# Kernel optimization log

Hardware: AMD Instinct MI355X
Metric: run time of the kernel (lower is better)

The kernel has to match this reference:

```python
import jax, jax.numpy as jnp
from jax import lax
import numpy as np

LEVELS = 17
VAR_N = 4
UNITS = 3 * LEVELS          # 51 neurons: motor 17, command 13, inter 21
MOTOR = LEVELS
PRED_N = 4
UNFOLDS = 6                 # ncps LTC default ode_unfolds
EPS = 1e-8
B = 32768                   # recurrence length = B + PRED_N
D = VAR_N * LEVELS          # 68


def _build_wiring(seed=0):
    # AutoNCP(51, 17, sparsity_level=0.8): inter=21, command=13, motor=17
    # sensory_fanout=4, inter_fanout=2, 5 recurrent command synapses, motor_fanin=2
    rng = np.random.default_rng(seed)
    motor, command, S = 17, 13, LEVELS
    N = UNITS
    cmd = np.arange(motor, motor + command)
    intr = np.arange(motor + command, N)
    adj = np.zeros((N, N), np.float32)
    sadj = np.zeros((S, N), np.float32)
    pol = lambda: float(rng.choice([-1.0, 1.0]))
    for s in range(S):
        for d in rng.choice(intr, 4, replace=False):
            sadj[s, d] = pol()
    for d in intr:
        if not sadj[:, d].any():
            sadj[int(rng.integers(S)), d] = pol()
    for i in intr:
        for d in rng.choice(cmd, 2, replace=False):
            adj[i, d] = pol()
    for d in cmd:
        if not adj[intr, d].any():
            adj[int(rng.choice(intr)), d] = pol()
    for _ in range(5):
        adj[int(rng.choice(cmd)), int(rng.choice(cmd))] = pol()
    for m in range(motor):
        for srci in rng.choice(cmd, 2, replace=False):
            adj[srci, m] = pol()
    return adj, sadj


def setup_inputs():
    key = jax.random.key(0)
    ks = iter(jax.random.split(key, 48))
    u = lambda s, lo, hi: jax.random.uniform(next(ks), s, jnp.float32, lo, hi)
    lin = lambda i, o: jax.random.normal(next(ks), (i, o), jnp.float32) * (i ** -0.5)
    adj, sadj = _build_wiring()
    V, N, S = VAR_N, UNITS, LEVELS
    M1 = (LEVELS + D) // 2           # 42
    G = VAR_N * D                    # 272
    G2 = (G + D) // 2                # 170
    return dict(
        x=jax.random.normal(next(ks), (B, D), jnp.float32),
        pre_w1=lin(D, D), pre_b1=jnp.zeros((D,), jnp.float32),
        pre_w2=lin(D, D), pre_b2=jnp.zeros((D,), jnp.float32),
        gleak=u((V, N), 0.001, 1.0), vleak=u((V, N), -0.2, 0.2), cm=u((V, N), 0.4, 0.6),
        w=u((V, N, N), 0.001, 1.0), sigma=u((V, N, N), 3.0, 8.0), mu=u((V, N, N), 0.3, 0.8),
        erev=jnp.asarray(np.tile(adj, (V, 1, 1))),
        sens_w=u((V, S, N), 0.001, 1.0), sens_sigma=u((V, S, N), 3.0, 8.0), sens_mu=u((V, S, N), 0.3, 0.8),
        sens_erev=jnp.asarray(np.tile(sadj, (V, 1, 1))),
        in_w=jnp.ones((V, S), jnp.float32), in_b=jnp.zeros((V, S), jnp.float32),
        out_w=jnp.ones((V, MOTOR), jnp.float32), out_b=jnp.zeros((V, MOTOR), jnp.float32),
        tW1=lin(LEVELS, LEVELS), tb1=jnp.zeros((LEVELS,), jnp.float32),
        tW2=lin(LEVELS, M1), tb2=jnp.zeros((M1,), jnp.float32),
        tW3=lin(M1, D), tb3=jnp.zeros((D,), jnp.float32),
        gW1=lin(G, G), gb1=jnp.zeros((G,), jnp.float32),
        gW2=lin(G, G2), gb2=jnp.zeros((G2,), jnp.float32),
        gW3=lin(G2, D), gb3=jnp.zeros((D,), jnp.float32),
        mask=jnp.asarray((adj != 0).astype(np.float32)),
        sens_mask=jnp.asarray((sadj != 0).astype(np.float32)),
    )


def _forward(x, pre_w1, pre_b1, pre_w2, pre_b2,
             gleak, vleak, cm, w, sigma, mu, erev,
             sens_w, sens_sigma, sens_mu, sens_erev,
             in_w, in_b, out_w, out_b,
             tW1, tb1, tW2, tb2, tW3, tb3,
             gW1, gb1, gW2, gb2, gW3, gb3,
             mask, sens_mask, ckpt=False):
    sig = jax.nn.sigmoid
    # VarEncoder: Linear -> Sigmoid -> Linear
    h = sig(x @ pre_w1 + pre_b1) @ pre_w2 + pre_b2                  # (B, 68)
    xs = h.reshape(-1, VAR_N, LEVELS).transpose(1, 0, 2)            # (V, B, 17)
    seqs = jnp.concatenate([xs, jnp.repeat(xs[:, -1:, :], PRED_N, axis=1)], axis=1)  # (V, T, 17)

    def run(p, seq):
        gl_, vl_, cm_, w_, sg_, mu_, er_, sw_, ssg_, smu_, ser_, iw_, ib_, ow_, ob_ = p
        gl = jax.nn.softplus(gl_)                 # (N,)
        wp = jax.nn.softplus(w_) * mask           # (N, N) sparse NCP wiring
        swp = jax.nn.softplus(sw_) * sens_mask    # (S, N)
        cmt = jax.nn.softplus(cm_) * UNFOLDS      # cm / (elapsed=1 / unfolds)

        def step(v, u_in):
            u = u_in * iw_ + ib_                                   # affine input mapping
            sact = swp * sig((u[:, None] - smu_) * ssg_)           # (S, N)
            num_s = (sact * ser_).sum(0)
            den_s = sact.sum(0)

            def unfold(vv, _):
                wa = wp * sig((vv[:, None] - mu_) * sg_)           # (N, N), src axis 0
                vv = (cmt * vv + gl * vl_ + (wa * er_).sum(0) + num_s) / (
                    cmt + gl + wa.sum(0) + den_s + EPS)
                return vv, None

            v, _ = lax.scan(unfold, v, None, length=UNFOLDS)
            return v, v[:MOTOR] * ow_ + ob_                        # affine output mapping

        stepf = jax.checkpoint(step) if ckpt else step
        _, outs = lax.scan(stepf, jnp.zeros((UNITS,), seq.dtype), seq)
        return outs                                                # (T, 17)

    p = (gleak, vleak, cm, w, sigma, mu, erev,
         sens_w, sens_sigma, sens_mu, sens_erev, in_w, in_b, out_w, out_b)
    rs = jax.vmap(run, in_axes=(0, 0))(p, seqs)                    # (V, T, 17)
    r = rs.transpose(1, 0, 2)                                      # (T, V, 17)
    # CrossConnector: per-tile MLP 17->17->42->68 (sigmoids), flatten, 272->272->170->68
    t = sig(sig(sig(r @ tW1 + tb1) @ tW2 + tb2) @ tW3 + tb3)        # (T, V, 68)
    g = t.reshape(t.shape[0], -1)                                   # (T, 272)
    return sig(sig(g @ gW1 + gb1) @ gW2 + gb2) @ gW3 + gb3          # (T, 68)


def reference(x, pre_w1, pre_b1, pre_w2, pre_b2,
              gleak, vleak, cm, w, sigma, mu, erev,
              sens_w, sens_sigma, sens_mu, sens_erev,
              in_w, in_b, out_w, out_b,
              tW1, tb1, tW2, tb2, tW3, tb3,
              gW1, gb1, gW2, gb2, gW3, gb3,
              mask, sens_mask):
    return _forward(x, pre_w1, pre_b1, pre_w2, pre_b2,
                    gleak, vleak, cm, w, sigma, mu, erev,
                    sens_w, sens_sigma, sens_mu, sens_erev,
                    in_w, in_b, out_w, out_b,
                    tW1, tb1, tW2, tb2, tW3, tb3,
                    gW1, gb1, gW2, gb2, gW3, gb3,
                    mask, sens_mask)
```

## Files before the change

### kernel.cpp

```cpp
#include <hip/hip_runtime.h>
#include <hip/hip_bf16.h>
#include <math.h>

#define LEVELS 17
#define VARN   4
#define UNITS  51
#define MOTOR  17
#define NB     32768
#define TT     (NB + 4)
#define DD     68
#define LOG2E  1.4426950408889634f
#define TROWS  16

#define W_WARM  10
#define L_CHUNK 34
#define NCHUNK  ((TT + L_CHUNK - 1) / L_CHUNK)

#define W_F     64
#define L_F     64
#define NCHUNK_F ((TT + L_F - 1) / L_F)
#define CAP_R  16

#define MROWS  48
#define MBLK   ((TT + MROWS - 1) / MROWS)
#define EBLK   ((NB + MROWS - 1) / MROWS)
#define BUFSZ  (48 * 272 + 64)
#define EBUFSZ (48 * 72 + 64)

#define OFF_WA 0
#define OFF_WB 7680
#define OFF_WC 24576
#define OFF_WD 76800
#define OFF_WE 155136
#define OFF_WF 205824
#define OFF_P1 221184
#define OFF_P2 228864
#define WTS_SHORTS 236544
#define PSENS_N (VARN * LEVELS * UNITS)

typedef __attribute__((ext_vector_type(8))) short short8v;
typedef __attribute__((ext_vector_type(4))) float f32x4;

__device__ __forceinline__ float fast_rcp(float x) { return __builtin_amdgcn_rcpf(x); }
__device__ __forceinline__ float fast_exp2(float x) { return __builtin_amdgcn_exp2f(x); }
__device__ __forceinline__ float sigf(float x) { return fast_rcp(1.0f + __expf(-x)); }
__device__ __forceinline__ float softplusf(float x) { return logf(1.0f + expf(x)); }
__device__ __forceinline__ unsigned short f2bf(float x) {
    unsigned int u = __float_as_uint(x);
    unsigned int r = u + 0x7FFFu + ((u >> 16) & 1u);
    return (unsigned short)(r >> 16);
}

__global__ __launch_bounds__(256) void prep_weights(
    const float* __restrict__ tW1, const float* __restrict__ tW2, const float* __restrict__ tW3,
    const float* __restrict__ gW1, const float* __restrict__ gW2, const float* __restrict__ gW3,
    const float* __restrict__ pW1, const float* __restrict__ pW2,
    unsigned short* __restrict__ wts)
{
    const int ph = blockIdx.y;
    const int KTt[8]   = {3, 3, 6, 9, 9, 6, 3, 3};
    const int NCt[8]   = {5, 11, 17, 17, 11, 5, 5, 5};
    const int offsT[8] = {OFF_WA, OFF_WB, OFF_WC, OFF_WD, OFF_WE, OFF_WF, OFF_P1, OFF_P2};
    int S = NCt[ph] * KTt[ph] * 512;
    int idx = blockIdx.x * 256 + threadIdx.x;
    if (idx >= S) return;
    int tile = idx >> 9;
    int r    = idx & 511;
    int lane = r >> 3;
    int e    = r & 7;
    int KTp  = KTt[ph];
    int ct   = tile / KTp;
    int kt   = tile - ct * KTp;
    int n = ct * 16 + (lane & 15);
    int k = kt * 32 + (lane >> 4) * 8 + e;
    float val = 0.0f;
    switch (ph) {
        case 0: if (k < 68 && n < 68) { int v = k / 17; if (n / 17 == v) val = tW1[(k % 17) * 17 + (n % 17)]; } break;
        case 1: if (k < 68 && n < 168) { int v = k / 17; int c = n - 42 * v; if (c >= 0 && c < 42) val = tW2[(k % 17) * 42 + c]; } break;
        case 2: if (k < 168 && n < 272) { int v = k / 42; int c = n - 68 * v; if (c >= 0 && c < 68) val = tW3[(k % 42) * 68 + c]; } break;
        case 3: if (k < 272 && n < 272) val = gW1[k * 272 + n]; break;
        case 4: if (k < 272 && n < 170) val = gW2[k * 170 + n]; break;
        case 5: if (k < 170 && n < 68)  val = gW3[k * 68 + n]; break;
        case 6: if (k < 68 && n < 68)   val = pW1[k * 68 + n]; break;
        case 7: if (k < 68 && n < 68)   val = pW2[k * 68 + n]; break;
    }
    wts[offsT[ph] + idx] = f2bf(val);
}

__global__ __launch_bounds__(256) void prep_sens(
    const float* __restrict__ sens_w, const float* __restrict__ sens_sigma,
    const float* __restrict__ sens_mu, const float* __restrict__ sens_erev,
    float4* __restrict__ psens)
{
    int idx = blockIdx.x * 256 + threadIdx.x;
    if (idx >= PSENS_N) return;
    float sg = sens_sigma[idx], m = sens_mu[idx];
    float wf = softplusf(sens_w[idx]);
    psens[idx] = make_float4(fast_exp2(sg * m * LOG2E), -sg * LOG2E, wf, wf * sens_erev[idx]);
}

template<int KT, int NC>
__device__ __forceinline__ void mfma_phase(
    const unsigned short* __restrict__ wt,
    const unsigned short* __restrict__ bufIn, int ldkIn,
    unsigned short* __restrict__ bufOut, int ldkOut,
    const float* __restrict__ bias, int bmod, int Nvalid,
    int lane, int wave)
{
    #pragma unroll
    for (int rt = 0; rt < 3; ++rt) {
        short8v af[KT];
        int abase = (rt * 16 + (lane & 15)) * ldkIn + 8 * (lane >> 4);
        #pragma unroll
        for (int kt = 0; kt < KT; ++kt)
            af[kt] = *reinterpret_cast<const short8v*>(&bufIn[abase + kt * 32]);
        for (int ct = wave; ct < NC; ct += 4) {
            int c = ct * 16 + (lane & 15);
            const unsigned short* wp = wt + (size_t)(ct * KT) * 512 + lane * 8;
            short8v bf[KT];
            #pragma unroll
            for (int kt = 0; kt < KT; ++kt)
                bf[kt] = *reinterpret_cast<const short8v*>(&wp[kt * 512]);
            f32x4 acc = {0.0f, 0.0f, 0.0f, 0.0f};
            #pragma unroll
            for (int kt = 0; kt < KT; ++kt)
                acc = __builtin_amdgcn_mfma_f32_16x16x32_bf16(af[kt], bf[kt], acc, 0, 0, 0);
            float bv = 0.0f;
            if (c < Nvalid) {
                int cb = (bmod == 0) ? (c % 17) : (bmod == 1) ? (c % 42) : (bmod == 2) ? (c % 68) : c;
                bv = bias[cb];
            }
            #pragma unroll
            for (int i = 0; i < 4; ++i) {
                float vv = sigf(acc[i] + bv);
                int rl = rt * 16 + (lane >> 4) * 4 + i;
                if (c < ldkOut) bufOut[rl * ldkOut + c] = f2bf(vv);
            }
        }
    }
}

template<int KT>
__device__ __forceinline__ void mfma_final(
    const unsigned short* __restrict__ wt,
    const unsigned short* __restrict__ bufIn, int ldkIn,
    float* __restrict__ io, int baseRow,
    const float* __restrict__ gb3, int lane, int wave)
{
    #pragma unroll
    for (int rt = 0; rt < 3; ++rt) {
        short8v af[KT];
        int abase = (rt * 16 + (lane & 15)) * ldkIn + 8 * (lane >> 4);
        #pragma unroll
        for (int kt = 0; kt < KT; ++kt)
            af[kt] = *reinterpret_cast<const short8v*>(&bufIn[abase + kt * 32]);
        for (int ct = wave; ct < 5; ct += 4) {
            int c = ct * 16 + (lane & 15);
            const unsigned short* wp = wt + (size_t)(ct * KT) * 512 + lane * 8;
            short8v bf[KT];
            #pragma unroll
            for (int kt = 0; kt < KT; ++kt)
                bf[kt] = *reinterpret_cast<const short8v*>(&wp[kt * 512]);
            f32x4 acc = {0.0f, 0.0f, 0.0f, 0.0f};
            #pragma unroll
            for (int kt = 0; kt < KT; ++kt)
                acc = __builtin_amdgcn_mfma_f32_16x16x32_bf16(af[kt], bf[kt], acc, 0, 0, 0);
            float bv = (c < 68) ? gb3[c] : 0.0f;
            #pragma unroll
            for (int i = 0; i < 4; ++i) {
                int row = baseRow + rt * 16 + (lane >> 4) * 4 + i;
                if (c < 68 && row < TT) io[(size_t)row * DD + c] = acc[i] + bv;
            }
        }
    }
}

__global__ __launch_bounds__(256) void mlp_mfma(
    float* __restrict__ io, const unsigned short* __restrict__ wts,
    const float* __restrict__ tb1, const float* __restrict__ tb2, const float* __restrict__ tb3,
    const float* __restrict__ gb1, const float* __restrict__ gb2, const float* __restrict__ gb3)
{
    __shared__ unsigned short buf0[BUFSZ];
    __shared__ unsigned short buf1[BUFSZ];
    int tid = threadIdx.x, lane = tid & 63, wave = tid >> 6;
    int baseRow = blockIdx.x * MROWS;

    for (int e = tid; e < BUFSZ; e += 256) { buf0[e] = 0; buf1[e] = 0; }
    __syncthreads();
    for (int e = tid; e < MROWS * DD; e += 256) {
        int r = e / DD, c = e % DD;
        int gr = baseRow + r;
        float xv = (gr < TT) ? io[(size_t)gr * DD + c] : 0.0f;
        buf0[r * 72 + c] = f2bf(xv);
    }
    __syncthreads();
    mfma_phase<3, 5 >(wts + OFF_WA, buf0, 72,  buf1, 72,  tb1, 0, 68,  lane, wave); __syncthreads();
    mfma_phase<3, 11>(wts + OFF_WB, buf1, 72,  buf0, 168, tb2, 1, 168, lane, wave); __syncthreads();
    mfma_phase<6, 17>(wts + OFF_WC, buf0, 168, buf1, 272, tb3, 2, 272, lane, wave); __syncthreads();
    mfma_phase<9, 17>(wts + OFF_WD, buf1, 272, buf0, 272, gb1, 3, 272, lane, wave); __syncthreads();
    mfma_phase<9, 11>(wts + OFF_WE, buf0, 272, buf1, 176, gb2, 3, 170, lane, wave); __syncthreads();
    mfma_final<6>(wts + OFF_WF, buf1, 176, io, baseRow, gb3, lane, wave);
}

__global__ __launch_bounds__(256) void enc_mfma(
    const float* __restrict__ x, const unsigned short* __restrict__ wts,
    const float* __restrict__ pb1, const float* __restrict__ pb2,
    float* __restrict__ seq)
{
    __shared__ unsigned short buf0[EBUFSZ];
    __shared__ unsigned short buf1[EBUFSZ];
    int tid = threadIdx.x, lane = tid & 63, wave = tid >> 6;
    int baseRow = blockIdx.x * MROWS;

    for (int e = tid; e < EBUFSZ; e += 256) { buf0[e] = 0; buf1[e] = 0; }
    __syncthreads();
    for (int e = tid; e < MROWS * DD; e += 256) {
        int r = e / DD, c = e % DD;
        int gr = baseRow + r;
        float xv = (gr < NB) ? x[(size_t)gr * DD + c] : 0.0f;
        buf0[r * 72 + c] = f2bf(xv);
    }
    __syncthreads();
    mfma_phase<3, 5>(wts + OFF_P1, buf0, 72, buf1, 72, pb1, 3, 68, lane, wave);
    __syncthreads();
    #pragma unroll
    for (int rt = 0; rt < 3; ++rt) {
        short8v af[3];
        int abase = (rt * 16 + (lane & 15)) * 72 + 8 * (lane >> 4);
        #pragma unroll
        for (int kt = 0; kt < 3; ++kt)
            af[kt] = *reinterpret_cast<const short8v*>(&buf1[abase + kt * 32]);
        for (int ct = wave; ct < 5; ct += 4) {
            int c = ct * 16 + (lane & 15);
            const unsigned short* wp = wts + OFF_P2 + (size_t)(ct * 3) * 512 + lane * 8;
            short8v bf[3];
            #pragma unroll
            for (int kt = 0; kt < 3; ++kt)
                bf[kt] = *reinterpret_cast<const short8v*>(&wp[kt * 512]);
            f32x4 acc = {0.0f, 0.0f, 0.0f, 0.0f};
            #pragma unroll
            for (int kt = 0; kt < 3; ++kt)
                acc = __builtin_amdgcn_mfma_f32_16x16x32_bf16(af[kt], bf[kt], acc, 0, 0, 0);
            float bv = (c < 68) ? pb2[c] : 0.0f;
            #pragma unroll
            for (int i = 0; i < 4; ++i) {
                int row = baseRow + rt * 16 + (lane >> 4) * 4 + i;
                if (c < 68 && row < NB) {
                    float vv = acc[i] + bv;
                    int v = c / 17, s = c % 17;
                    float* dst = seq + ((size_t)v * TT + row) * LEVELS + s;
                    dst[0] = vv;
                    if (row == NB - 1) {
                        dst[1 * LEVELS] = vv; dst[2 * LEVELS] = vv;
                        dst[3 * LEVELS] = vv; dst[4 * LEVELS] = vv;
                    }
                }
            }
        }
    }
}

#define SENS_TPW 16
__global__ __launch_bounds__(256) void sens_kernel(
    const float* __restrict__ seq,
    const float4* __restrict__ psens,
    const float* __restrict__ in_w, const float* __restrict__ in_b,
    const float* __restrict__ sens_mask,
    float2* __restrict__ tab)
{
    int gwi = blockIdx.x * 4 + (threadIdx.x >> 6);
    int j   = threadIdx.x & 63;
    int v    = gwi & 3;
    int tbase = (gwi >> 2) * SENS_TPW;
    if (tbase >= TT) return;

    unsigned int bits0 = 0;
    if (j < UNITS)
        for (int s = 0; s < LEVELS; ++s)
            bits0 |= (sens_mask[s * UNITS + j] != 0.0f ? 1u : 0u) << s;
    int ns = __popc(bits0);
    int mS = ns;
    #pragma unroll
    for (int off = 32; off; off >>= 1) mS = max(mS, __shfl_xor(mS, off, 64));

    float iw = (j < LEVELS) ? in_w[v * LEVELS + j] : 0.0f;
    float ib = (j < LEVELS) ? in_b[v * LEVELS + j] : 0.0f;

    int tend = min(TT, tbase + SENS_TPW);
    for (int t = tbase; t < tend; ++t) {
        float u = (j < LEVELS)
            ? fmaf(seq[((size_t)v * TT + t) * LEVELS + j], iw, ib) : 0.0f;
        unsigned int bits = bits0;
        float num = 0.0f, den = 0.0f;
        for (int k = 0; k < mS; ++k) {
            bool on = (k < ns) && (bits != 0u);
            int s = on ? (__ffs(bits) - 1) : 0;
            if (on) bits &= bits - 1;
            float us = __shfl(u, s, 64);
            float4 p = psens[(v * LEVELS + s) * UNITS + (j < UNITS ? j : 0)];
            float g = fast_rcp(fmaf(p.x, fast_exp2(p.y * us), 1.0f));
            if (on) { num = fmaf(p.w, g, num); den = fmaf(p.z, g, den); }
        }
        if (j < UNITS)
            tab[((size_t)v * TT + t) * UNITS + j] = make_float2(num, den);
    }
}

template<int MH>
__device__ void scan_body3(
    int j, int jnS, int jnV, float ownMul, float helpMul, int h1, int h2,
    int myStart, int myCnt, bool isH1,
    unsigned long long colbits, int v, int t0, int wstart, int tend,
    float cmt, float glvl, float cgl, float ow, float ob,
    const float* __restrict__ w, const float* __restrict__ sigma,
    const float* __restrict__ mu, const float* __restrict__ erev,
    const float2* __restrict__ tab, float* __restrict__ rout)
{
    int   src[MH]; float fw[MH], fc[MH], fk[MH], fwfe[MH];
    unsigned long long bits = colbits;
    for (int s = 0; s < myStart; ++s) bits &= bits - 1;
    #pragma unroll
    for (int k = 0; k < MH; ++k) {
        bool on = (k < myCnt);
        int sc = on ? (__ffsll((unsigned long long)bits) - 1) : 0;
        src[k] = sc;
        size_t pi = ((size_t)v * UNITS + sc) * UNITS + jnS;
        float sg = on ? sigma[pi] : 0.0f;
        float m  = on ? mu[pi]    : 0.0f;
        fw[k] = on ? softplusf(w[pi]) : 0.0f;
        fc[k] = fast_exp2(sg * m * LOG2E);
        fk[k] = -sg * LOG2E;
        fwfe[k] = on ? fw[k] * erev[pi] : 0.0f;
        if (on) bits &= bits - 1;
    }
    const float2* tp = tab + (size_t)v * TT * UNITS + jnV;
    float* rp = rout + (size_t)v * LEVELS + j;
    float2 nd = tp[(size_t)t0 * UNITS];
    float vreg = 0.0f;
    for (int t = t0; t < tend; ++t) {
        float2 ndc = nd;
        if (t + 1 < tend) nd = tp[(size_t)(t + 1) * UNITS];
        float bn = isH1 ? 0.0f : (glvl + ndc.x);
        float bd = isH1 ? 1.0f : (cgl + ndc.y);
        #pragma unroll
        for (int uf = 0; uf < 6; ++uf) {
            float vs[MH];
            #pragma unroll
            for (int k = 0; k < MH; ++k) vs[k] = __shfl(vreg, src[k], 64);
            float accn = 0.0f, accd = 0.0f;
            #pragma unroll
            for (int k = 0; k < MH; ++k) {
                float g = fast_rcp(fmaf(fc[k], fast_exp2(fk[k] * vs[k]), 1.0f));
                accn = fmaf(fwfe[k], g, accn);
                accd = fmaf(fw[k], g, accd);
            }
            float p1n = __shfl(accn, h1, 64);
            float p1d = __shfl(accd, h1, 64);
            float p2n = __shfl(accn, h2, 64);
            float p2d = __shfl(accd, h2, 64);
            float num = fmaf(accn, ownMul, bn) + helpMul * (p1n + p2n);
            float den = fmaf(accd, ownMul, bd) + helpMul * (p1d + p2d);
            vreg = fmaf(cmt, vreg, num) * fast_rcp(den);
        }
        if (j < MOTOR && t >= wstart) rp[(size_t)t * DD] = fmaf(vreg, ow, ob);
    }
}

__device__ void scan_body_gen(
    int j, int jn, bool hasHelp, int partner, int myStart, int myCnt, int mcMax,
    unsigned long long colbits, int v, int t0, int wstart, int tend,
    float cmt, float glvl, float cgl, float ow, float ob, bool isHelper,
    const float* __restrict__ w, const float* __restrict__ sigma,
    const float* __restrict__ mu, const float* __restrict__ erev,
    const float2* __restrict__ tab, float* __restrict__ rout)
{
    unsigned long long mybits = colbits;
    for (int s = 0; s < myStart; ++s) mybits &= mybits - 1;
    const float2* tp = tab + (size_t)v * TT * UNITS + jn;
    float* rp = rout + (size_t)v * LEVELS + j;
    float vreg = 0.0f;
    for (int t = t0; t < tend; ++t) {
        float2 ndc = tp[(size_t)t * UNITS];
        float bn = isHelper ? 0.0f : (glvl + ndc.x);
        float bd = isHelper ? 0.0f : (cgl + ndc.y);
        for (int uf = 0; uf < 6; ++uf) {
            unsigned long long bits = mybits;
            float num = bn, den = bd;
            for (int k = 0; k < mcMax; ++k) {
                bool on = (k < myCnt) && (bits != 0ull);
                int sc = on ? (__ffsll(bits) - 1) : 0;
                if (on) bits &= bits - 1;
                float vs = __shfl(vreg, sc, 64);
                size_t pi = ((size_t)v * UNITS + sc) * UNITS + jn;
                float a = on ? softplusf(w[pi]) * sigf((vs - mu[pi]) * sigma[pi]) : 0.0f;
                num = fmaf(a, on ? erev[pi] : 0.0f, num);
                den += a;
            }
            float pn = __shfl(num, partner, 64);
            float pd = __shfl(den, partner, 64);
            if (hasHelp) { num += pn; den += pd; }
            vreg = fmaf(cmt, vreg, num) * fast_rcp(den);
        }
        if (j < MOTOR && t >= wstart) rp[(size_t)t * DD] = fmaf(vreg, ow, ob);
    }
}

__global__ __launch_bounds__(256, 8) void scan_pre(
    const float2* __restrict__ tab,
    const float* __restrict__ gleak, const float* __restrict__ vleak, const float* __restrict__ cm,
    const float* __restrict__ w, const float* __restrict__ sigma,
    const float* __restrict__ mu, const float* __restrict__ erev,
    const float* __restrict__ out_w, const float* __restrict__ out_b,
    const float* __restrict__ mask,
    float* __restrict__ rout)
{
    int gwi = (blockIdx.x << 2) + (threadIdx.x >> 6);
    int j = threadIdx.x & 63;
    int v = gwi & 3;
    int chunk = gwi >> 2;
    if (chunk >= NCHUNK) return;
    int wstart = chunk * L_CHUNK;
    int tend = min(TT, wstart + L_CHUNK);
    int t0 = max(0, wstart - W_WARM);

    bool isH1   = (j >= UNITS);
    bool isH2   = (j >= 30 && j < 43);
    bool isCmdL = (j >= MOTOR && j < 30);
    int jnV = isH1 ? (j - 34) : j;
    int jnS = isH1 ? (j - 34) : (isH2 ? (j - 13) : j);

    unsigned long long colbits = 0ull;
    for (int i = 0; i < UNITS; ++i)
        colbits |= (unsigned long long)(mask[i * UNITS + jnS] != 0.0f ? 1 : 0) << i;
    int nf = __popcll(colbits);

    int ownIn = 0;
    if (j >= 30 && j < UNITS) {
        for (int i = 0; i < UNITS; ++i)
            ownIn |= (mask[i * UNITS + j] != 0.0f ? 1 : 0);
    }
    int bad = ownIn;
    #pragma unroll
    for (int off = 32; off; off >>= 1) bad |= __shfl_xor(bad, off, 64);

    int n1 = (nf + 2) / 3;
    int n2 = (nf - n1 + 1) / 2;
    int n3 = nf - n1 - n2;
    int myStart, myCnt;
    if (isH1)        { myStart = n1 + n2; myCnt = n3; }
    else if (isH2)   { myStart = n1;      myCnt = n2; }
    else if (isCmdL) { myStart = 0;       myCnt = n1; }
    else             { myStart = 0;       myCnt = nf; }
    float ownMul  = (isH1 || isH2) ? 0.0f : 1.0f;
    float helpMul = isCmdL ? 1.0f : 0.0f;
    int h1 = isCmdL ? (j + 34) : j;
    int h2 = isCmdL ? (j + 13) : j;

    float cmt  = softplusf(cm[v * UNITS + jnV]) * 6.0f;
    float gl   = softplusf(gleak[v * UNITS + jnV]);
    float glvl = gl * vleak[v * UNITS + jnV];
    float cgl  = cmt + gl + 1e-8f;
    float ow = (j < MOTOR) ? out_w[v * LEVELS + j] : 0.0f;
    float ob = (j < MOTOR) ? out_b[v * LEVELS + j] : 0.0f;

    int mc = myCnt;
    #pragma unroll
    for (int off = 32; off; off >>= 1) mc = max(mc, __shfl_xor(mc, off, 64));

    if (!bad && mc <= 2)
        scan_body3<2>(j, jnS, jnV, ownMul, helpMul, h1, h2, myStart, myCnt, isH1,
                      colbits, v, t0, wstart, tend, cmt, glvl, cgl, ow, ob,
                      w, sigma, mu, erev, tab, rout);
    else if (!bad && mc <= 3)
        scan_body3<3>(j, jnS, jnV, ownMul, helpMul, h1, h2, myStart, myCnt, isH1,
                      colbits, v, t0, wstart, tend, cmt, glvl, cgl, ow, ob,
                      w, sigma, mu, erev, tab, rout);
    else if (!bad && mc <= 4)
        scan_body3<4>(j, jnS, jnV, ownMul, helpMul, h1, h2, myStart, myCnt, isH1,
                      colbits, v, t0, wstart, tend, cmt, glvl, cgl, ow, ob,
                      w, sigma, mu, erev, tab, rout);
    else {
        int jn = isH1 ? (j - 34) : j;
        unsigned long long cb = 0ull;
        for (int i = 0; i < UNITS; ++i)
            cb |= (unsigned long long)(mask[i * UNITS + jn] != 0.0f ? 1 : 0) << i;
        int nfg = __popcll(cb);
        bool isCmd = (jn >= MOTOR && jn < 30);
        int nh = (nfg + 1) >> 1;
        int gs, gc;
        if (isH1)      { gs = nh; gc = nfg - nh; }
        else if (isCmd){ gs = 0;  gc = nh; }
        else           { gs = 0;  gc = nfg; }
        bool hasHelp = (!isH1) && isCmd;
        int partner = hasHelp ? (jn + 34) : j;
        float cmtg  = softplusf(cm[v * UNITS + jn]) * 6.0f;
        float glg   = softplusf(gleak[v * UNITS + jn]);
        float glvlg = glg * vleak[v * UNITS + jn];
        float cglg  = cmtg + glg + 1e-8f;
        int mg = gc;
        #pragma unroll
        for (int off = 32; off; off >>= 1) mg = max(mg, __shfl_xor(mg, off, 64));
        scan_body_gen(j, jn, hasHelp, partner, gs, gc, mg, cb, v, t0, wstart, tend,
                      cmtg, glvlg, cglg, ow, ob, isH1, w, sigma, mu, erev, tab, rout);
    }
}

__global__ __launch_bounds__(128) void enc_kernel(
    const float* __restrict__ x,
    const float* __restrict__ W1, const float* __restrict__ b1,
    const float* __restrict__ W2, const float* __restrict__ b2,
    float* __restrict__ seq)
{
    int t = blockIdx.x;
    int j = threadIdx.x;
    __shared__ float xs[DD];
    __shared__ float h1[DD];
    if (j < DD) xs[j] = x[(size_t)t * DD + j];
    __syncthreads();
    if (j < DD) {
        float acc = b1[j];
        #pragma unroll 4
        for (int k = 0; k < DD; ++k) acc = fmaf(xs[k], W1[k * DD + j], acc);
        h1[j] = sigf(acc);
    }
    __syncthreads();
    if (j < DD) {
        float acc = b2[j];
        #pragma unroll 4
        for (int k = 0; k < DD; ++k) acc = fmaf(h1[k], W2[k * DD + j], acc);
        int v = j / LEVELS, s = j % LEVELS;
        float* dst = seq + ((size_t)v * TT + t) * LEVELS + s;
        dst[0] = acc;
        if (t == NB - 1) {
            dst[1 * LEVELS] = acc; dst[2 * LEVELS] = acc;
            dst[3 * LEVELS] = acc; dst[4 * LEVELS] = acc;
        }
    }
}

template<int MF, int MS>
__device__ __forceinline__ void scan_loop_f(
    int j, int v, int t0, int wstart, int tend,
    const float* __restrict__ seq, float* __restrict__ rout,
    float cmt, float glvl, float cgl, float iw, float ib, float ow, float ob,
    int nf, int ns,
    const int* rs_, const float* rw_, const float* rc_, const float* rk_, const float* re_,
    const int* ss_, const float* sw_, const float* sc_, const float* sk_, const float* se_)
{
    int fs[MF]; float fw[MF], fc[MF], fk[MF], fe[MF];
    #pragma unroll
    for (int k = 0; k < MF; ++k) {
        bool on = k < nf;
        int idx = j * CAP_R + k;
        fs[k] = on ? rs_[idx] : 0;
        fw[k] = on ? rw_[idx] : 0.0f;
        fc[k] = on ? rc_[idx] : 1.0f;
        fk[k] = on ? rk_[idx] : 0.0f;
        fe[k] = on ? re_[idx] : 0.0f;
    }
    int gs[MS]; float gw[MS], gc[MS], gk[MS], ge[MS];
    #pragma unroll
    for (int k = 0; k < MS; ++k) {
        bool on = k < ns;
        int idx = j * LEVELS + k;
        gs[k] = on ? ss_[idx] : 0;
        gw[k] = on ? sw_[idx] : 0.0f;
        gc[k] = on ? sc_[idx] : 1.0f;
        gk[k] = on ? sk_[idx] : 0.0f;
        ge[k] = on ? se_[idx] : 0.0f;
    }
    const float* sp = seq + (size_t)v * TT * LEVELS + j;
    float* rp = rout + (size_t)v * LEVELS + j;
    float xnext = (j < LEVELS) ? sp[(size_t)t0 * LEVELS] : 0.0f;
    float vreg = 0.0f;
    for (int t = t0; t < tend; ++t) {
        float u = fmaf(xnext, iw, ib);
        if (j < LEVELS && t + 1 < tend) xnext = sp[(size_t)(t + 1) * LEVELS];
        float us[MS];
        #pragma unroll
        for (int k = 0; k < MS; ++k) us[k] = __shfl(u, gs[k], 64);
        float sa[MS];
        #pragma unroll
        for (int k = 0; k < MS; ++k)
            sa[k] = gw[k] * fast_rcp(fmaf(gc[k], fast_exp2(gk[k] * us[k]), 1.0f));
        float bn = glvl, bd = cgl;
        #pragma unroll
        for (int k = 0; k < MS; ++k) { bn = fmaf(sa[k], ge[k], bn); bd += sa[k]; }
        #pragma unroll
        for (int uf = 0; uf < 6; ++uf) {
            float vsa[MF];
            #pragma unroll
            for (int k = 0; k < MF; ++k) vsa[k] = __shfl(vreg, fs[k], 64);
            float aa[MF];
            #pragma unroll
            for (int k = 0; k < MF; ++k)
                aa[k] = fw[k] * fast_rcp(fmaf(fc[k], fast_exp2(fk[k] * vsa[k]), 1.0f));
            float num = bn, den = bd;
            #pragma unroll
            for (int k = 0; k < MF; ++k) { num = fmaf(aa[k], fe[k], num); den += aa[k]; }
            vreg = fmaf(cmt, vreg, num) * fast_rcp(den);
        }
        if (j < LEVELS && t >= wstart) rp[(size_t)t * DD] = fmaf(vreg, ow, ob);
    }
}

__global__ __launch_bounds__(64) void scan_fallback(
    const float* __restrict__ seq,
    const float* __restrict__ gleak, const float* __restrict__ vleak, const float* __restrict__ cm,
    const float* __restrict__ w, const float* __restrict__ sigma,
    const float* __restrict__ mu, const float* __restrict__ erev,
    const float* __restrict__ sens_w, const float* __restrict__ sens_sigma,
    const float* __restrict__ sens_mu, const float* __restrict__ sens_erev,
    const float* __restrict__ in_w, const float* __restrict__ in_b,
    const float* __restrict__ out_w, const float* __restrict__ out_b,
    const float* __restrict__ mask, const float* __restrict__ sens_mask,
    float* __restrict__ rout)
{
    __shared__ int   rs_[UNITS * CAP_R];
    __shared__ float rw_[UNITS * CAP_R], rc_[UNITS * CAP_R], rk_[UNITS * CAP_R], re_[UNITS * CAP_R];
    __shared__ int   ss_[UNITS * LEVELS];
    __shared__ float sw_[UNITS * LEVELS], sc_[UNITS * LEVELS], sk_[UNITS * LEVELS], se_[UNITS * LEVELS];
    __shared__ int   cnts[64], scnts[64];
    __shared__ int   red[2];

    int j = threadIdx.x;
    int v = blockIdx.x & 3;
    int chunk = blockIdx.x >> 2;
    int wstart = chunk * L_F;
    if (wstart >= TT) return;
    int tend = min(TT, wstart + L_F);
    int t0 = max(0, wstart - W_F);

    int nf = 0, ns = 0;
    if (j < UNITS) {
        for (int i = 0; i < UNITS; ++i) {
            if (mask[i * UNITS + j] != 0.0f) {
                if (nf < CAP_R) {
                    size_t pi = ((size_t)v * UNITS + i) * UNITS + j;
                    int idx = j * CAP_R + nf;
                    float sg = sigma[pi], m = mu[pi];
                    rs_[idx] = i;
                    rw_[idx] = softplusf(w[pi]);
                    rc_[idx] = fast_exp2(sg * m * LOG2E);
                    rk_[idx] = -sg * LOG2E;
                    re_[idx] = erev[pi];
                }
                nf++;
            }
        }
        for (int s = 0; s < LEVELS; ++s) {
            if (sens_mask[s * UNITS + j] != 0.0f) {
                size_t pi = ((size_t)v * LEVELS + s) * UNITS + j;
                int idx = j * LEVELS + ns;
                float sg = sens_sigma[pi], m = sens_mu[pi];
                ss_[idx] = s;
                sw_[idx] = softplusf(sens_w[pi]);
                sc_[idx] = fast_exp2(sg * m * LOG2E);
                sk_[idx] = -sg * LOG2E;
                se_[idx] = sens_erev[pi];
                ns++;
            }
        }
    }
    cnts[j] = nf; scnts[j] = ns;
    __syncthreads();
    if (j == 0) {
        int mf = 0, ms = 0;
        for (int i = 0; i < UNITS; ++i) { mf = max(mf, cnts[i]); ms = max(ms, scnts[i]); }
        red[0] = mf; red[1] = ms;
    }
    __syncthreads();
    int maxF = red[0], maxS = red[1];

    int jc = (j < UNITS) ? j : (UNITS - 1);
    float cmt  = softplusf(cm[v * UNITS + jc]) * 6.0f;
    float gl   = softplusf(gleak[v * UNITS + jc]);
    float glvl = gl * vleak[v * UNITS + jc];
    float cgl  = cmt + gl + 1e-8f;
    float iw = (j < LEVELS) ? in_w[v * LEVELS + j]  : 0.0f;
    float ib = (j < LEVELS) ? in_b[v * LEVELS + j]  : 0.0f;
    float ow = (j < LEVELS) ? out_w[v * LEVELS + j] : 0.0f;
    float ob = (j < LEVELS) ? out_b[v * LEVELS + j] : 0.0f;

    if (maxF <= 11 && maxS <= 12)
        scan_loop_f<11, 12>(j, v, t0, wstart, tend, seq, rout, cmt, glvl, cgl, iw, ib, ow, ob, nf, ns,
                            rs_, rw_, rc_, rk_, re_, ss_, sw_, sc_, sk_, se_);
    else
        scan_loop_f<16, 17>(j, v, t0, wstart, tend, seq, rout, cmt, glvl, cgl, iw, ib, ow, ob, nf, ns,
                            rs_, rw_, rc_, rk_, re_, ss_, sw_, sc_, sk_, se_);
}

__global__ __launch_bounds__(256) void mlp_kernel(
    float* __restrict__ io,
    const float* __restrict__ tW1, const float* __restrict__ tb1,
    const float* __restrict__ tW2, const float* __restrict__ tb2,
    const float* __restrict__ tW3, const float* __restrict__ tb3,
    const float* __restrict__ gW1, const float* __restrict__ gb1,
    const float* __restrict__ gW2, const float* __restrict__ gb2,
    const float* __restrict__ gW3, const float* __restrict__ gb3)
{
    __shared__ __align__(16) float A[TROWS][272];
    __shared__ __align__(16) float Bf[TROWS][272];
    int base = blockIdx.x * TROWS;
    int tid = threadIdx.x;

    for (int e = tid; e < TROWS * DD; e += 256) {
        int r = e / DD, c = e % DD;
        A[r][c] = (base + r < TT) ? io[(size_t)(base + r) * DD + c] : 0.0f;
    }
    __syncthreads();
    for (int c = tid; c < 4 * LEVELS; c += 256) {
        int vv = c / LEVELS, cc = c % LEVELS;
        float acc[TROWS]; float bias = tb1[cc];
        #pragma unroll
        for (int r = 0; r < TROWS; ++r) acc[r] = bias;
        for (int k = 0; k < LEVELS; ++k) {
            float wv = tW1[k * LEVELS + cc];
            #pragma unroll
            for (int r = 0; r < TROWS; ++r) acc[r] = fmaf(A[r][vv * LEVELS + k], wv, acc[r]);
        }
        #pragma unroll
        for (int r = 0; r < TROWS; ++r) Bf[r][c] = sigf(acc[r]);
    }
    __syncthreads();
    for (int c = tid; c < 4 * 42; c += 256) {
        int vv = c / 42, cc = c % 42;
        float acc[TROWS]; float bias = tb2[cc];
        #pragma unroll
        for (int r = 0; r < TROWS; ++r) acc[r] = bias;
        for (int k = 0; k < LEVELS; ++k) {
            float wv = tW2[k * 42 + cc];
            #pragma unroll
            for (int r = 0; r < TROWS; ++r) acc[r] = fmaf(Bf[r][vv * LEVELS + k], wv, acc[r]);
        }
        #pragma unroll
        for (int r = 0; r < TROWS; ++r) A[r][vv * 42 + cc] = sigf(acc[r]);
    }
    __syncthreads();
    for (int c = tid; c < 4 * DD; c += 256) {
        int vv = c / DD, cc = c % DD;
        float acc[TROWS]; float bias = tb3[cc];
        #pragma unroll
        for (int r = 0; r < TROWS; ++r) acc[r] = bias;
        for (int k = 0; k < 42; ++k) {
            float wv = tW3[k * DD + cc];
            #pragma unroll
            for (int r = 0; r < TROWS; ++r) acc[r] = fmaf(A[r][vv * 42 + k], wv, acc[r]);
        }
        #pragma unroll
        for (int r = 0; r < TROWS; ++r) Bf[r][c] = sigf(acc[r]);
    }
    __syncthreads();
    for (int c = tid; c < 272; c += 256) {
        float acc[TROWS]; float bias = gb1[c];
        #pragma unroll
        for (int r = 0; r < TROWS; ++r) acc[r] = bias;
        for (int k = 0; k < 272; k += 4) {
            float w0 = gW1[(k + 0) * 272 + c];
            float w1 = gW1[(k + 1) * 272 + c];
            float w2 = gW1[(k + 2) * 272 + c];
            float w3 = gW1[(k + 3) * 272 + c];
            #pragma unroll
            for (int r = 0; r < TROWS; ++r) {
                float4 g4 = *reinterpret_cast<const float4*>(&Bf[r][k]);
                acc[r] = fmaf(g4.x, w0, fmaf(g4.y, w1, fmaf(g4.z, w2, fmaf(g4.w, w3, acc[r]))));
            }
        }
        #pragma unroll
        for (int r = 0; r < TROWS; ++r) A[r][c] = sigf(acc[r]);
    }
    __syncthreads();
    for (int c = tid; c < 170; c += 256) {
        float acc[TROWS]; float bias = gb2[c];
        #pragma unroll
        for (int r = 0; r < TROWS; ++r) acc[r] = bias;
        for (int k = 0; k < 272; k += 4) {
            float w0 = gW2[(k + 0) * 170 + c];
            float w1 = gW2[(k + 1) * 170 + c];
            float w2 = gW2[(k + 2) * 170 + c];
            float w3 = gW2[(k + 3) * 170 + c];
            #pragma unroll
            for (int r = 0; r < TROWS; ++r) {
                float4 g4 = *reinterpret_cast<const float4*>(&A[r][k]);
                acc[r] = fmaf(g4.x, w0, fmaf(g4.y, w1, fmaf(g4.z, w2, fmaf(g4.w, w3, acc[r]))));
            }
        }
        #pragma unroll
        for (int r = 0; r < TROWS; ++r) Bf[r][c] = sigf(acc[r]);
    }
    __syncthreads();
    for (int c = tid; c < DD; c += 256) {
        float acc[TROWS]; float bias = gb3[c];
        #pragma unroll
        for (int r = 0; r < TROWS; ++r) acc[r] = bias;
        for (int k = 0; k < 168; k += 4) {
            float w0 = gW3[(k + 0) * DD + c];
            float w1 = gW3[(k + 1) * DD + c];
            float w2 = gW3[(k + 2) * DD + c];
            float w3 = gW3[(k + 3) * DD + c];
            #pragma unroll
            for (int r = 0; r < TROWS; ++r) {
                float4 g4 = *reinterpret_cast<const float4*>(&Bf[r][k]);
                acc[r] = fmaf(g4.x, w0, fmaf(g4.y, w1, fmaf(g4.z, w2, fmaf(g4.w, w3, acc[r]))));
            }
        }
        for (int k = 168; k < 170; ++k) {
            float wv = gW3[k * DD + c];
            #pragma unroll
            for (int r = 0; r < TROWS; ++r) acc[r] = fmaf(Bf[r][k], wv, acc[r]);
        }
        #pragma unroll
        for (int r = 0; r < TROWS; ++r)
            if (base + r < TT) io[(size_t)(base + r) * DD + c] = acc[r];
    }
}

extern "C" void kernel_launch(void* const* d_in, const int* in_sizes, int n_in,
                              void* d_out, int out_size, void* d_ws, size_t ws_size,
                              hipStream_t stream)
{
    (void)in_sizes; (void)n_in; (void)out_size;
    const float* x        = (const float*)d_in[0];
    const float* pre_w1   = (const float*)d_in[1];
    const float* pre_b1   = (const float*)d_in[2];
    const float* pre_w2   = (const float*)d_in[3];
    const float* pre_b2   = (const float*)d_in[4];
    const float* gleak    = (const float*)d_in[5];
    const float* vleak    = (const float*)d_in[6];
    const float* cm       = (const float*)d_in[7];
    const float* w        = (const float*)d_in[8];
    const float* sigma    = (const float*)d_in[9];
    const float* mu       = (const float*)d_in[10];
    const float* erev     = (const float*)d_in[11];
    const float* sens_w   = (const float*)d_in[12];
    const float* sens_sig = (const float*)d_in[13];
    const float* sens_mu  = (const float*)d_in[14];
    const float* sens_er  = (const float*)d_in[15];
    const float* in_w     = (const float*)d_in[16];
    const float* in_b     = (const float*)d_in[17];
    const float* out_w    = (const float*)d_in[18];
    const float* out_b    = (const float*)d_in[19];
    const float* tW1      = (const float*)d_in[20];
    const float* tb1      = (const float*)d_in[21];
    const float* tW2      = (const float*)d_in[22];
    const float* tb2      = (const float*)d_in[23];
    const float* tW3      = (const float*)d_in[24];
    const float* tb3      = (const float*)d_in[25];
    const float* gW1      = (const float*)d_in[26];
    const float* gb1      = (const float*)d_in[27];
    const float* gW2      = (const float*)d_in[28];
    const float* gb2      = (const float*)d_in[29];
    const float* gW3      = (const float*)d_in[30];
    const float* gb3      = (const float*)d_in[31];
    const float* mask     = (const float*)d_in[32];
    const float* smask    = (const float*)d_in[33];

    float* out = (float*)d_out;

    size_t tab_bytes = (size_t)VARN * TT * UNITS * sizeof(float2);
    size_t seq_bytes = (size_t)VARN * TT * LEVELS * sizeof(float);
    size_t wts_bytes = (size_t)WTS_SHORTS * sizeof(unsigned short);
    size_t ps_bytes  = (size_t)PSENS_N * sizeof(float4);

    if (ws_size >= tab_bytes + seq_bytes + wts_bytes + ps_bytes) {
        float2* tab = (float2*)d_ws;
        float*  seq = (float*)((char*)d_ws + tab_bytes);
        unsigned short* wts = (unsigned short*)((char*)d_ws + tab_bytes + seq_bytes);
        float4* psens = (float4*)((char*)d_ws + tab_bytes + seq_bytes + wts_bytes);
        prep_weights<<<dim3(306, 8), 256, 0, stream>>>(
            tW1, tW2, tW3, gW1, gW2, gW3, pre_w1, pre_w2, wts);
        prep_sens<<<(PSENS_N + 255) / 256, 256, 0, stream>>>(
            sens_w, sens_sig, sens_mu, sens_er, psens);
        enc_mfma<<<EBLK, 256, 0, stream>>>(x, wts, pre_b1, pre_b2, seq);
        {
            int slabs = (TT + SENS_TPW - 1) / SENS_TPW;
            int waves = slabs * VARN;
            sens_kernel<<<(waves + 3) / 4, 256, 0, stream>>>(
                seq, psens, in_w, in_b, smask, tab);
        }
        scan_pre<<<NCHUNK, 256, 0, stream>>>(
            tab, gleak, vleak, cm, w, sigma, mu, erev, out_w, out_b, mask, out);
        mlp_mfma<<<MBLK, 256, 0, stream>>>(out, wts, tb1, tb2, tb3, gb1, gb2, gb3);
    } else if (ws_size >= seq_bytes) {
        float* seq = (float*)d_ws;
        enc_kernel<<<NB, 128, 0, stream>>>(x, pre_w1, pre_b1, pre_w2, pre_b2, seq);
        scan_fallback<<<VARN * NCHUNK_F, 64, 0, stream>>>(
            seq, gleak, vleak, cm, w, sigma, mu, erev,
            sens_w, sens_sig, sens_mu, sens_er,
            in_w, in_b, out_w, out_b, mask, smask, out);
        mlp_kernel<<<(TT + TROWS - 1) / TROWS, 256, 0, stream>>>(
            out, tW1, tb1, tW2, tb2, tW3, tb3, gW1, gb1, gW2, gb2, gW3, gb3);
    }
}
```

Before: 225.7 us.

## Fuse sensory table computation into encoder and merge prep kernels

Merges the weight and sensory-parameter prep kernels into one launch. The sensory synapse table is now computed directly inside the encoder MFMA kernel from shared memory, so the intermediate sequence buffer is no longer written and re-read. This cuts launch overhead and global memory traffic. The scan chunk length is also increased, reducing warmup overhead per chunk at the cost of fewer parallel chunks.

```diff
diff --git a/kernel.cpp b/kernel.cpp
--- a/kernel.cpp
+++ b/kernel.cpp
@@ -13,7 +13,7 @@
 #define TROWS  16
 
 #define W_WARM  10
-#define L_CHUNK 34
+#define L_CHUNK 40
 #define NCHUNK  ((TT + L_CHUNK - 1) / L_CHUNK)
 
 #define W_F     64
@@ -51,13 +51,23 @@
     return (unsigned short)(r >> 16);
 }
 
-__global__ __launch_bounds__(256) void prep_weights(
+__global__ __launch_bounds__(256) void prep_all(
     const float* __restrict__ tW1, const float* __restrict__ tW2, const float* __restrict__ tW3,
     const float* __restrict__ gW1, const float* __restrict__ gW2, const float* __restrict__ gW3,
     const float* __restrict__ pW1, const float* __restrict__ pW2,
-    unsigned short* __restrict__ wts)
+    const float* __restrict__ sens_w, const float* __restrict__ sens_sigma,
+    const float* __restrict__ sens_mu, const float* __restrict__ sens_erev,
+    unsigned short* __restrict__ wts, float4* __restrict__ psens)
 {
     const int ph = blockIdx.y;
+    if (ph == 8) {
+        int idx = blockIdx.x * 256 + threadIdx.x;
+        if (idx >= PSENS_N) return;
+        float sg = sens_sigma[idx], m = sens_mu[idx];
+        float wf = softplusf(sens_w[idx]);
+        psens[idx] = make_float4(fast_exp2(sg * m * LOG2E), -sg * LOG2E, wf, wf * sens_erev[idx]);
+        return;
+    }
     const int KTt[8]   = {3, 3, 6, 9, 9, 6, 3, 3};
     const int NCt[8]   = {5, 11, 17, 17, 11, 5, 5, 5};
     const int offsT[8] = {OFF_WA, OFF_WB, OFF_WC, OFF_WD, OFF_WE, OFF_WF, OFF_P1, OFF_P2};
@@ -87,18 +97,6 @@
     wts[offsT[ph] + idx] = f2bf(val);
 }
 
-__global__ __launch_bounds__(256) void prep_sens(
-    const float* __restrict__ sens_w, const float* __restrict__ sens_sigma,
-    const float* __restrict__ sens_mu, const float* __restrict__ sens_erev,
-    float4* __restrict__ psens)
-{
-    int idx = blockIdx.x * 256 + threadIdx.x;
-    if (idx >= PSENS_N) return;
-    float sg = sens_sigma[idx], m = sens_mu[idx];
-    float wf = softplusf(sens_w[idx]);
-    psens[idx] = make_float4(fast_exp2(sg * m * LOG2E), -sg * LOG2E, wf, wf * sens_erev[idx]);
-}
-
 template<int KT, int NC>
 __device__ __forceinline__ void mfma_phase(
     const unsigned short* __restrict__ wt,
@@ -205,14 +203,25 @@
 __global__ __launch_bounds__(256) void enc_mfma(
     const float* __restrict__ x, const unsigned short* __restrict__ wts,
     const float* __restrict__ pb1, const float* __restrict__ pb2,
-    float* __restrict__ seq)
+    const float4* __restrict__ psens,
+    const float* __restrict__ in_w, const float* __restrict__ in_b,
+    const float* __restrict__ sens_mask,
+    float2* __restrict__ tab)
 {
     __shared__ unsigned short buf0[EBUFSZ];
     __shared__ unsigned short buf1[EBUFSZ];
+    __shared__ float usf[MROWS][DD];
+    __shared__ unsigned int sbits[UNITS];
     int tid = threadIdx.x, lane = tid & 63, wave = tid >> 6;
     int baseRow = blockIdx.x * MROWS;
 
     for (int e = tid; e < EBUFSZ; e += 256) { buf0[e] = 0; buf1[e] = 0; }
+    if (tid < UNITS) {
+        unsigned int b = 0;
+        for (int s = 0; s < LEVELS; ++s)
+            b |= (sens_mask[s * UNITS + tid] != 0.0f ? 1u : 0u) << s;
+        sbits[tid] = b;
+    }
     __syncthreads();
     for (int e = tid; e < MROWS * DD; e += 256) {
         int r = e / DD, c = e % DD;
@@ -241,68 +250,40 @@
             #pragma unroll
             for (int kt = 0; kt < 3; ++kt)
                 acc = __builtin_amdgcn_mfma_f32_16x16x32_bf16(af[kt], bf[kt], acc, 0, 0, 0);
-            float bv = (c < 68) ? pb2[c] : 0.0f;
-            #pragma unroll
-            for (int i = 0; i < 4; ++i) {
-                int row = baseRow + rt * 16 + (lane >> 4) * 4 + i;
-                if (c < 68 && row < NB) {
-                    float vv = acc[i] + bv;
-                    int v = c / 17, s = c % 17;
-                    float* dst = seq + ((size_t)v * TT + row) * LEVELS + s;
-                    dst[0] = vv;
-                    if (row == NB - 1) {
-                        dst[1 * LEVELS] = vv; dst[2 * LEVELS] = vv;
-                        dst[3 * LEVELS] = vv; dst[4 * LEVELS] = vv;
-                    }
+            if (c < 68) {
+                float bv = pb2[c];
+                float iw = in_w[c], ib = in_b[c];
+                #pragma unroll
+                for (int i = 0; i < 4; ++i) {
+                    int rl = rt * 16 + (lane >> 4) * 4 + i;
+                    usf[rl][c] = fmaf(acc[i] + bv, iw, ib);
                 }
             }
         }
     }
-}
-
-#define SENS_TPW 16
-__global__ __launch_bounds__(256) void sens_kernel(
-    const float* __restrict__ seq,
-    const float4* __restrict__ psens,
-    const float* __restrict__ in_w, const float* __restrict__ in_b,
-    const float* __restrict__ sens_mask,
-    float2* __restrict__ tab)
-{
-    int gwi = blockIdx.x * 4 + (threadIdx.x >> 6);
-    int j   = threadIdx.x & 63;
-    int v    = gwi & 3;
-    int tbase = (gwi >> 2) * SENS_TPW;
-    if (tbase >= TT) return;
-
-    unsigned int bits0 = 0;
-    if (j < UNITS)
-        for (int s = 0; s < LEVELS; ++s)
-            bits0 |= (sens_mask[s * UNITS + j] != 0.0f ? 1u : 0u) << s;
-    int ns = __popc(bits0);
-    int mS = ns;
-    #pragma unroll
-    for (int off = 32; off; off >>= 1) mS = max(mS, __shfl_xor(mS, off, 64));
-
-    float iw = (j < LEVELS) ? in_w[v * LEVELS + j] : 0.0f;
-    float ib = (j < LEVELS) ? in_b[v * LEVELS + j] : 0.0f;
-
-    int tend = min(TT, tbase + SENS_TPW);
-    for (int t = tbase; t < tend; ++t) {
-        float u = (j < LEVELS)
-            ? fmaf(seq[((size_t)v * TT + t) * LEVELS + j], iw, ib) : 0.0f;
-        unsigned int bits = bits0;
+    __syncthreads();
+    for (int e = tid; e < MROWS * VARN * UNITS; e += 256) {
+        int r = e / (VARN * UNITS);
+        int rem = e - r * (VARN * UNITS);
+        int v = rem / UNITS;
+        int j = rem - v * UNITS;
+        int grow = baseRow + r;
+        if (grow >= NB) continue;
+        unsigned int bits = sbits[j];
         float num = 0.0f, den = 0.0f;
-        for (int k = 0; k < mS; ++k) {
-            bool on = (k < ns) && (bits != 0u);
-            int s = on ? (__ffs(bits) - 1) : 0;
-            if (on) bits &= bits - 1;
-            float us = __shfl(u, s, 64);
-            float4 p = psens[(v * LEVELS + s) * UNITS + (j < UNITS ? j : 0)];
-            float g = fast_rcp(fmaf(p.x, fast_exp2(p.y * us), 1.0f));
-            if (on) { num = fmaf(p.w, g, num); den = fmaf(p.z, g, den); }
-        }
-        if (j < UNITS)
-            tab[((size_t)v * TT + t) * UNITS + j] = make_float2(num, den);
+        while (bits) {
+            int s = __ffs(bits) - 1; bits &= bits - 1;
+            float4 p = psens[(v * LEVELS + s) * UNITS + j];
+            float g = fast_rcp(fmaf(p.x, fast_exp2(p.y * usf[r][v * LEVELS + s]), 1.0f));
+            num = fmaf(p.w, g, num);
+            den = fmaf(p.z, g, den);
+        }
+        size_t o = ((size_t)v * TT + grow) * UNITS + j;
+        tab[o] = make_float2(num, den);
+        if (grow == NB - 1) {
+            #pragma unroll
+            for (int k = 1; k <= 4; ++k) tab[o + (size_t)k * UNITS] = make_float2(num, den);
+        }
     }
 }
 
@@ -864,20 +845,13 @@
 
     if (ws_size >= tab_bytes + seq_bytes + wts_bytes + ps_bytes) {
         float2* tab = (float2*)d_ws;
-        float*  seq = (float*)((char*)d_ws + tab_bytes);
         unsigned short* wts = (unsigned short*)((char*)d_ws + tab_bytes + seq_bytes);
         float4* psens = (float4*)((char*)d_ws + tab_bytes + seq_bytes + wts_bytes);
-        prep_weights<<<dim3(306, 8), 256, 0, stream>>>(
-            tW1, tW2, tW3, gW1, gW2, gW3, pre_w1, pre_w2, wts);
-        prep_sens<<<(PSENS_N + 255) / 256, 256, 0, stream>>>(
-            sens_w, sens_sig, sens_mu, sens_er, psens);
-        enc_mfma<<<EBLK, 256, 0, stream>>>(x, wts, pre_b1, pre_b2, seq);
-        {
-            int slabs = (TT + SENS_TPW - 1) / SENS_TPW;
-            int waves = slabs * VARN;
-            sens_kernel<<<(waves + 3) / 4, 256, 0, stream>>>(
-                seq, psens, in_w, in_b, smask, tab);
-        }
+        prep_all<<<dim3(306, 9), 256, 0, stream>>>(
+            tW1, tW2, tW3, gW1, gW2, gW3, pre_w1, pre_w2,
+            sens_w, sens_sig, sens_mu, sens_er, wts, psens);
+        enc_mfma<<<EBLK, 256, 0, stream>>>(
+            x, wts, pre_b1, pre_b2, psens, in_w, in_b, smask, tab);
         scan_pre<<<NCHUNK, 256, 0, stream>>>(
             tab, gleak, vleak, cm, w, sigma, mu, erev, out_w, out_b, mask, out);
         mlp_mfma<<<MBLK, 256, 0, stream>>>(out, wts, tb1, tb2, tb3, gb1, gb2, gb3);
```

Result: slower. 240.0 us (+6.3%).
